# Optimization experiments

Measured on AMD Instinct MI355X. Metric: run time of the kernel, lower is better.

The kernel has to match this reference:

```python
import jax, jax.numpy as jnp
import numpy as np

B, S, H, HEADS = 4, 2048, 512, 8
DK = H // HEADS
LN_EPS = 1e-5
NEG_INF = -1e30


def setup_inputs() -> dict:
    key = jax.random.key(0)
    k = jax.random.split(key, 6)
    x = jax.random.normal(k[0], (B, S, H), dtype=jnp.float32)
    mask = jax.random.randint(k[1], (B, S), 0, 2, dtype=jnp.int32)
    # per-head Q/K/V projection weights stacked: [heads, H, dk]
    Wq = jax.random.normal(k[2], (HEADS, H, DK), dtype=jnp.float32) * 0.05
    Wk = jax.random.normal(k[3], (HEADS, H, DK), dtype=jnp.float32) * 0.05
    Wv = jax.random.normal(k[4], (HEADS, H, DK), dtype=jnp.float32) * 0.05
    # output projection: [heads*dk, H] (y = h @ Wo)
    Wo = jax.random.normal(k[5], (HEADS * DK, H), dtype=jnp.float32) * 0.05
    gamma = jnp.ones((H,), dtype=jnp.float32)
    beta = jnp.zeros((H,), dtype=jnp.float32)
    return {"x": x, "mask": mask, "Wq": Wq, "Wk": Wk, "Wv": Wv,
            "Wo": Wo, "gamma": gamma, "beta": beta}


def reference(x, mask, Wq, Wk, Wv, Wo, gamma, beta):
    # LayerNorm over hidden dim
    mu = jnp.mean(x, axis=-1, keepdims=True)
    var = jnp.mean(jnp.square(x - mu), axis=-1, keepdims=True)
    xn = (x - mu) * jax.lax.rsqrt(var + LN_EPS) * gamma + beta  # [B,S,H]

    mf = mask.astype(jnp.float32)  # [B,S]

    # batched per-head projections (original loops over heads)
    q = jnp.einsum('bsh,nhd->bnsd', xn, Wq)  # [B,heads,S,dk]
    kk = jnp.einsum('bsh,nhd->bnsd', xn, Wk)
    v = jnp.einsum('bsh,nhd->bnsd', xn, Wv)

    scores = jnp.einsum('bnqd,bnkd->bnqk', q, kk) / np.sqrt(DK).astype(np.float32)
    m = mf[:, None, None, :]  # [B,1,1,S] broadcast over query dim
    logits = m * scores + (1.0 - m) * NEG_INF
    probs = jax.nn.softmax(logits, axis=-1)
    attn = jnp.einsum('bnqk,bnkd->bnqd', probs, v)  # [B,heads,S,dk]

    h = attn.transpose(0, 2, 1, 3).reshape(x.shape[0], x.shape[1], HEADS * DK)
    out = h @ Wo + xn          # residual adds post-norm x (as in original)
    out = out * mf[:, :, None]  # zero out masked positions
    return out
```

## Files before the change

kernel.cpp:

```cpp
#include <hip/hip_runtime.h>
#include <hip/hip_bf16.h>
#include <math.h>

#define B_ 4
#define S_ 2048
#define H_ 512
#define HEADS_ 8
#define DK_ 64
#define NROWS_ (B_*S_)
#define LN_EPS_ 1e-5f
#define NEG_INF_ -1e30f
#define QSCALE_ (0.125f * 1.44269504088896f)

typedef short s8v __attribute__((ext_vector_type(8)));
typedef short s4v __attribute__((ext_vector_type(4)));
typedef float f4v __attribute__((ext_vector_type(4)));

typedef __attribute__((address_space(1))) unsigned int gu32_t;
typedef __attribute__((address_space(3))) unsigned int lu32_t;

__device__ __forceinline__ unsigned short f2bf(float f) {
    unsigned int u = __float_as_uint(f);
    u += 0x7FFFu + ((u >> 16) & 1u);
    return (unsigned short)(u >> 16);
}

__device__ __forceinline__ float bf2f(unsigned short u) {
    return __uint_as_float((unsigned int)u << 16);
}

__device__ __forceinline__ s4v pk4bf(float a, float b, float c, float d) {
    union { __hip_bfloat162 h[2]; s4v v; } u;
    u.h[0] = __float22bfloat162_rn(float2{a, b});
    u.h[1] = __float22bfloat162_rn(float2{c, d});
    return u.v;
}

__global__ __launch_bounds__(256) void prep_kernel(
        const float* __restrict__ x, const float* __restrict__ gamma,
        const float* __restrict__ beta, const int* __restrict__ mask,
        const float* __restrict__ Wq, const float* __restrict__ Wk,
        const float* __restrict__ Wv, const float* __restrict__ Wo,
        unsigned short* __restrict__ xnb, float* __restrict__ mb,
        unsigned short* __restrict__ Wt) {
    int bx = blockIdx.x;
    if (bx < 2048) {
        int row  = bx * 4 + (threadIdx.x >> 6);
        int lane = threadIdx.x & 63;
        const float4* xr = (const float4*)(x + (size_t)row * H_ + lane * 8);
        float4 a = xr[0], d = xr[1];
        float s  = (a.x + a.y) + (a.z + a.w) + (d.x + d.y) + (d.z + d.w);
        float ss = (a.x*a.x + a.y*a.y) + (a.z*a.z + a.w*a.w)
                 + (d.x*d.x + d.y*d.y) + (d.z*d.z + d.w*d.w);
        #pragma unroll
        for (int i = 1; i < 64; i <<= 1) {
            s  += __shfl_xor(s, i, 64);
            ss += __shfl_xor(ss, i, 64);
        }
        float mu  = s * (1.f / 512.f);
        float var = ss * (1.f / 512.f) - mu * mu;
        float rstd = rsqrtf(var + LN_EPS_);
        if (lane == 0) mb[row] = mask[row] ? 0.f : NEG_INF_;
        const float4* gp = (const float4*)(gamma + lane * 8);
        const float4* bp = (const float4*)(beta + lane * 8);
        float4 g0 = gp[0], g1 = gp[1], b0 = bp[0], b1 = bp[1];
        float4 y0, y1;
        y0.x = (a.x - mu) * rstd * g0.x + b0.x;
        y0.y = (a.y - mu) * rstd * g0.y + b0.y;
        y0.z = (a.z - mu) * rstd * g0.z + b0.z;
        y0.w = (a.w - mu) * rstd * g0.w + b0.w;
        y1.x = (d.x - mu) * rstd * g1.x + b1.x;
        y1.y = (d.y - mu) * rstd * g1.y + b1.y;
        y1.z = (d.z - mu) * rstd * g1.z + b1.z;
        y1.w = (d.w - mu) * rstd * g1.w + b1.w;
        union { s4v h[2]; s8v v; } pk;
        pk.h[0] = pk4bf(y0.x, y0.y, y0.z, y0.w);
        pk.h[1] = pk4bf(y1.x, y1.y, y1.z, y1.w);
        *(s8v*)(xnb + (size_t)row * H_ + lane * 8) = pk.v;
    } else {
        __shared__ float tile[32][33];
        int wid = bx - 2048;
        const float* src;
        int ld, drow, k0, c0;
        float scale = 1.f;
        if (wid < 768) {
            int z = wid >> 5, rem = wid & 31;
            int cx = rem & 1, ky = rem >> 1;
            k0 = ky * 32; c0 = cx * 32;
            int zw = z >> 3, head = z & 7;
            const float* W = (zw == 0) ? Wq : (zw == 1) ? Wk : Wv;
            if (zw == 0) scale = QSCALE_;
            src = W + (size_t)head * H_ * DK_;
            ld = DK_;
            drow = zw * 512 + head * 64;
        } else {
            int rem = wid - 768;
            int cx = rem & 15, ky = rem >> 4;
            k0 = ky * 32; c0 = cx * 32;
            src = Wo; ld = H_; drow = 1536;
        }
        int tx = threadIdx.x & 31, ty = threadIdx.x >> 5;
        #pragma unroll
        for (int i = 0; i < 4; i++)
            tile[ty * 4 + i][tx] = src[(size_t)(k0 + ty * 4 + i) * ld + c0 + tx];
        __syncthreads();
        #pragma unroll
        for (int i = 0; i < 4; i++) {
            int cc = ty * 4 + i;
            Wt[(size_t)(drow + c0 + cc) * 512 + k0 + tx] = f2bf(tile[tx][cc] * scale);
        }
    }
}

__device__ __forceinline__ void gemm_tile(
        const unsigned short* __restrict__ A,
        const unsigned short* __restrict__ Bt,
        int r0, int j0, f4v acc[4][4]) {
    __shared__ unsigned short As[3 * 128 * 32];
    __shared__ unsigned short Bs[3 * 128 * 32];
    int t = threadIdx.x;
    int wv = t >> 6, L = t & 63, c = L & 15, g = L >> 4;
    int m_base = (wv & 1) * 64, n_base = (wv >> 1) * 64;
    #pragma unroll
    for (int i = 0; i < 4; i++)
        #pragma unroll
        for (int j = 0; j < 4; j++) acc[i][j] = (f4v){0.f, 0.f, 0.f, 0.f};

    auto stage = [&](int buf, int k0) {
        #pragma unroll
        for (int i = 0; i < 2; i++) {
            int uu = wv * 128 + i * 64 + L;
            int row = uu >> 2, k16 = uu & 3;
            __builtin_amdgcn_global_load_lds(
                (const gu32_t*)(A + (size_t)(r0 + row) * 512 + k0 + k16 * 8),
                (lu32_t*)(As + buf * 4096 + (size_t)(wv * 128 + i * 64) * 8), 16, 0, 0);
            __builtin_amdgcn_global_load_lds(
                (const gu32_t*)(Bt + (size_t)(j0 + row) * 512 + k0 + k16 * 8),
                (lu32_t*)(Bs + buf * 4096 + (size_t)(wv * 128 + i * 64) * 8), 16, 0, 0);
        }
    };

    auto compute = [&](int buf) {
        s8v a[4], b[4];
        #pragma unroll
        for (int i = 0; i < 4; i++)
            a[i] = *(const s8v*)(As + buf * 4096 + (size_t)(m_base + i * 16 + c) * 32 + g * 8);
        #pragma unroll
        for (int j = 0; j < 4; j++)
            b[j] = *(const s8v*)(Bs + buf * 4096 + (size_t)(n_base + j * 16 + c) * 32 + g * 8);
        #pragma unroll
        for (int i = 0; i < 4; i++)
            #pragma unroll
            for (int j = 0; j < 4; j++)
                acc[i][j] = __builtin_amdgcn_mfma_f32_16x16x32_bf16(
                    a[i], b[j], acc[i][j], 0, 0, 0);
    };

    stage(0, 0);
    stage(1, 32);
    #pragma unroll
    for (int s = 0; s < 14; ++s) {
        stage((s + 2) % 3, (s + 2) * 32);
        __asm__ volatile("s_waitcnt vmcnt(8)" ::: "memory");
        __builtin_amdgcn_s_barrier();
        compute(s % 3);
        __builtin_amdgcn_s_barrier();
    }
    __asm__ volatile("s_waitcnt vmcnt(4)" ::: "memory");
    __builtin_amdgcn_s_barrier();
    compute(14 % 3);
    __builtin_amdgcn_s_barrier();
    __asm__ volatile("s_waitcnt vmcnt(0)" ::: "memory");
    __builtin_amdgcn_s_barrier();
    compute(15 % 3);
}

__global__ __launch_bounds__(256) void qkv_gemm(
        const unsigned short* __restrict__ xnb,
        const unsigned short* __restrict__ Wt,
        unsigned short* __restrict__ Qb, unsigned short* __restrict__ Kf,
        unsigned short* __restrict__ Vf) {
    f4v acc[4][4];
    int t = threadIdx.x;
    int wv = t >> 6, L = t & 63, c = L & 15, g = L >> 4;
    int rb = wv & 1, cb = wv >> 1;
    if (blockIdx.x < 8) {
        int m0 = blockIdx.x * 128, n0 = blockIdx.y * 128;
        gemm_tile(Wt, xnb, m0, n0, acc);
        int R0 = m0 + rb * 64;
        int C0 = n0 + cb * 64;
        int hd = (R0 >> 6) & 7;
        int b  = C0 >> 11, srow0 = C0 & 2047;
        size_t bhbase = (size_t)(b * HEADS_ + hd) * S_ * DK_;
        if (R0 < 512) {
            #pragma unroll
            for (int msub = 0; msub < 4; msub++) {
                int dk4 = msub * 16 + g * 4;
                #pragma unroll
                for (int nsub = 0; nsub < 4; nsub++) {
                    int tok = srow0 + nsub * 16 + c;
                    s4v v = pk4bf(acc[msub][nsub][0], acc[msub][nsub][1],
                                  acc[msub][nsub][2], acc[msub][nsub][3]);
                    *(s4v*)(Qb + bhbase + (size_t)tok * DK_ + dk4) = v;
                }
            }
        } else {
            unsigned short* dst = Kf + bhbase + (size_t)(srow0 >> 6) * 4096;
            #pragma unroll
            for (int msub = 0; msub < 4; msub++) {
                int gx = (msub & 1) * 2 + (g >> 1);
                int slotbase = (g & 1) * 4 + (msub >> 1) * 8;
                #pragma unroll
                for (int nsub = 0; nsub < 4; nsub++) {
                    s4v v = pk4bf(acc[msub][nsub][0], acc[msub][nsub][1],
                                  acc[msub][nsub][2], acc[msub][nsub][3]);
                    *(s4v*)(dst + nsub * 1024 + (gx * 16 + c) * 16 + slotbase) = v;
                }
            }
        }
    } else {
        int r0 = blockIdx.y * 128, j0 = 1024 + (blockIdx.x - 8) * 128;
        gemm_tile(xnb, Wt, r0, j0, acc);
        int R0 = r0 + rb * 64;
        int C0 = j0 + cb * 64;
        int hd = (C0 >> 6) & 7;
        int b = R0 >> 11, srow0 = R0 & 2047;
        unsigned short* dst = Vf + (size_t)(b * HEADS_ + hd) * S_ * DK_
                              + (size_t)(srow0 >> 6) * 4096;
        #pragma unroll
        for (int msub = 0; msub < 4; msub++)
            #pragma unroll
            for (int nsub = 0; nsub < 4; nsub++) {
                s4v v = pk4bf(acc[msub][nsub][0], acc[msub][nsub][1],
                              acc[msub][nsub][2], acc[msub][nsub][3]);
                *(s4v*)(dst + nsub * 1024 + (g * 16 + c) * 16 + msub * 4) = v;
            }
    }
}

struct KHalf {
    s8v k0lo, k0hi, k1lo, k1hi;
    float4 mb0, mb1;
};

__global__ __launch_bounds__(256, 3) void attn_kernel(
        const unsigned short* __restrict__ Qb,
        const unsigned short* __restrict__ Kf,
        const unsigned short* __restrict__ Vf,
        const float* __restrict__ mb,
        unsigned short* __restrict__ hb) {
    __shared__ float red[2][64][2][17];

    int wv   = threadIdx.x >> 6;
    int qsub = wv & 1;
    int kp   = wv >> 1;
    int L  = threadIdx.x & 63;
    int c  = L & 15;
    int g  = L >> 4;

    unsigned wgid = blockIdx.x + blockIdx.y * 32u;
    unsigned xcd  = wgid & 7u;
    unsigned idx  = wgid >> 3;
    int bh = (int)(xcd + (idx >> 5) * 8u);
    int qt = (int)(idx & 31u);
    int b  = bh >> 3, n = bh & 7;
    int q0 = qt * 64 + qsub * 32;

    const unsigned short* Qbase = Qb + (size_t)bh * S_ * DK_;
    const unsigned short* Kp = Kf + (size_t)bh * S_ * DK_ + (size_t)kp * 16 * 4096 + L * 16;
    const unsigned short* Vp = Vf + (size_t)bh * S_ * DK_ + (size_t)kp * 16 * 4096 + L * 16;
    const float* mbrow = mb + b * S_ + kp * 1024;

    s8v qfA0 = *(const s8v*)(Qbase + (size_t)(q0 + c) * DK_ + g * 8);
    s8v qfA1 = *(const s8v*)(Qbase + (size_t)(q0 + c) * DK_ + 32 + g * 8);
    s8v qfB0 = *(const s8v*)(Qbase + (size_t)(q0 + 16 + c) * DK_ + g * 8);
    s8v qfB1 = *(const s8v*)(Qbase + (size_t)(q0 + 16 + c) * DK_ + 32 + g * 8);

    f4v accA[4], accB[4];
    #pragma unroll
    for (int i = 0; i < 4; i++) {
        accA[i] = (f4v){0.f, 0.f, 0.f, 0.f};
        accB[i] = (f4v){0.f, 0.f, 0.f, 0.f};
    }
    float lacA[4] = {0.f, 0.f, 0.f, 0.f};
    float lacB[4] = {0.f, 0.f, 0.f, 0.f};

    auto load_kh = [&](int kb, int h, KHalf& d) {
        const unsigned short* Kn = Kp + (size_t)kb * 4096;
        d.k0lo = *(const s8v*)(Kn + (h * 2 + 0) * 1024);
        d.k0hi = *(const s8v*)(Kn + (h * 2 + 0) * 1024 + 8);
        d.k1lo = *(const s8v*)(Kn + (h * 2 + 1) * 1024);
        d.k1hi = *(const s8v*)(Kn + (h * 2 + 1) * 1024 + 8);
        d.mb0  = *(const float4*)(mbrow + kb * 64 + h * 32 + g * 4);
        d.mb1  = *(const float4*)(mbrow + kb * 64 + h * 32 + 16 + g * 4);
    };

    auto compute_half = [&](const KHalf& d, int kb, int h) {
        const unsigned short* Vn = Vp + (size_t)kb * 4096;
        s8v vv[4];
        #pragma unroll
        for (int ds = 0; ds < 4; ds++)
            vv[ds] = *(const s8v*)(Vn + ds * 1024 + h * 8);
        f4v bias0 = (f4v){d.mb0.x, d.mb0.y, d.mb0.z, d.mb0.w};
        f4v bias1 = (f4v){d.mb1.x, d.mb1.y, d.mb1.z, d.mb1.w};
        f4v sA0 = bias0, sA1 = bias1, sB0 = bias0, sB1 = bias1;
        sA0 = __builtin_amdgcn_mfma_f32_16x16x32_bf16(d.k0lo, qfA0, sA0, 0, 0, 0);
        sA0 = __builtin_amdgcn_mfma_f32_16x16x32_bf16(d.k0hi, qfA1, sA0, 0, 0, 0);
        sA1 = __builtin_amdgcn_mfma_f32_16x16x32_bf16(d.k1lo, qfA0, sA1, 0, 0, 0);
        sA1 = __builtin_amdgcn_mfma_f32_16x16x32_bf16(d.k1hi, qfA1, sA1, 0, 0, 0);
        sB0 = __builtin_amdgcn_mfma_f32_16x16x32_bf16(d.k0lo, qfB0, sB0, 0, 0, 0);
        sB0 = __builtin_amdgcn_mfma_f32_16x16x32_bf16(d.k0hi, qfB1, sB0, 0, 0, 0);
        sB1 = __builtin_amdgcn_mfma_f32_16x16x32_bf16(d.k1lo, qfB0, sB1, 0, 0, 0);
        sB1 = __builtin_amdgcn_mfma_f32_16x16x32_bf16(d.k1hi, qfB1, sB1, 0, 0, 0);
        float pA0[4], pA1[4], pB0[4], pB1[4];
        #pragma unroll
        for (int r = 0; r < 4; r++) {
            pA0[r] = __builtin_amdgcn_exp2f(sA0[r]);
            pA1[r] = __builtin_amdgcn_exp2f(sA1[r]);
            pB0[r] = __builtin_amdgcn_exp2f(sB0[r]);
            pB1[r] = __builtin_amdgcn_exp2f(sB1[r]);
            lacA[r] += pA0[r] + pA1[r];
            lacB[r] += pB0[r] + pB1[r];
        }
        s4v pfA0 = pk4bf(pA0[0], pA0[1], pA0[2], pA0[3]);
        s4v pfA1 = pk4bf(pA1[0], pA1[1], pA1[2], pA1[3]);
        s4v pfB0 = pk4bf(pB0[0], pB0[1], pB0[2], pB0[3]);
        s4v pfB1 = pk4bf(pB1[0], pB1[1], pB1[2], pB1[3]);
        #pragma unroll
        for (int ds = 0; ds < 4; ds++) {
            s4v v0 = __builtin_shufflevector(vv[ds], vv[ds], 0, 1, 2, 3);
            s4v v1 = __builtin_shufflevector(vv[ds], vv[ds], 4, 5, 6, 7);
            accA[ds] = __builtin_amdgcn_mfma_f32_16x16x16bf16_1k(v0, pfA0, accA[ds], 0, 0, 0);
            accA[ds] = __builtin_amdgcn_mfma_f32_16x16x16bf16_1k(v1, pfA1, accA[ds], 0, 0, 0);
            accB[ds] = __builtin_amdgcn_mfma_f32_16x16x16bf16_1k(v0, pfB0, accB[ds], 0, 0, 0);
            accB[ds] = __builtin_amdgcn_mfma_f32_16x16x16bf16_1k(v1, pfB1, accB[ds], 0, 0, 0);
        }
    };

    KHalf ha, hb2;
    load_kh(0, 0, ha);
    for (int kb = 0; kb < 16; kb++) {
        load_kh(kb, 1, hb2);
        compute_half(ha, kb, 0);
        int kbn = (kb < 15) ? kb + 1 : 15;
        load_kh(kbn, 0, ha);
        compute_half(hb2, kb, 1);
    }

    float lA = (lacA[0] + lacA[1]) + (lacA[2] + lacA[3]);
    float lB = (lacB[0] + lacB[1]) + (lacB[2] + lacB[3]);
    lA += __shfl_xor(lA, 16, 64);
    lA += __shfl_xor(lA, 32, 64);
    lB += __shfl_xor(lB, 16, 64);
    lB += __shfl_xor(lB, 32, 64);

    if (kp == 1) {
        #pragma unroll
        for (int d = 0; d < 4; d++) {
            #pragma unroll
            for (int r = 0; r < 4; r++) {
                red[qsub][L][0][d * 4 + r] = accA[d][r];
                red[qsub][L][1][d * 4 + r] = accB[d][r];
            }
        }
        red[qsub][L][0][16] = lA;
        red[qsub][L][1][16] = lB;
    }
    __syncthreads();
    if (kp == 0) {
        const float* srcA = &red[qsub][L][0][0];
        const float* srcB = &red[qsub][L][1][0];
        float invA = 1.f / (lA + srcA[16]);
        float invB = 1.f / (lB + srcB[16]);
        unsigned short* hpA = hb + (size_t)(b * S_ + q0 + c) * H_ + n * DK_ + g * 4;
        unsigned short* hpB = hpA + (size_t)16 * H_;
        #pragma unroll
        for (int ds = 0; ds < 4; ds++) {
            s4v oA = pk4bf((accA[ds][0] + srcA[ds * 4 + 0]) * invA,
                           (accA[ds][1] + srcA[ds * 4 + 1]) * invA,
                           (accA[ds][2] + srcA[ds * 4 + 2]) * invA,
                           (accA[ds][3] + srcA[ds * 4 + 3]) * invA);
            *(s4v*)(hpA + ds * 16) = oA;
            s4v oB = pk4bf((accB[ds][0] + srcB[ds * 4 + 0]) * invB,
                           (accB[ds][1] + srcB[ds * 4 + 1]) * invB,
                           (accB[ds][2] + srcB[ds * 4 + 2]) * invB,
                           (accB[ds][3] + srcB[ds * 4 + 3]) * invB);
            *(s4v*)(hpB + ds * 16) = oB;
        }
    }
}

__global__ __launch_bounds__(256) void out_gemm(
        const unsigned short* __restrict__ hb,
        const unsigned short* __restrict__ Wot,
        const unsigned short* __restrict__ xnb, const int* __restrict__ mask,
        float* __restrict__ out) {
    f4v acc[4][4];
    int r0 = blockIdx.y * 128, j0 = blockIdx.x * 128;
    gemm_tile(hb, Wot, r0, j0, acc);
    int t = threadIdx.x;
    int wv = t >> 6, L = t & 63, c = L & 15, g = L >> 4;
    int mrow = r0 + (wv & 1) * 64 + g * 4;
    int ncol = j0 + (wv >> 1) * 64 + c;
    #pragma unroll
    for (int msub = 0; msub < 4; msub++) {
        #pragma unroll
        for (int rr = 0; rr < 4; rr++) {
            int row = mrow + msub * 16 + rr;
            float mf = (float)mask[row];
            #pragma unroll
            for (int nsub = 0; nsub < 4; nsub++) {
                int col = ncol + nsub * 16;
                size_t o = (size_t)row * H_ + col;
                out[o] = (acc[msub][nsub][rr] + bf2f(xnb[o])) * mf;
            }
        }
    }
}

extern "C" void kernel_launch(void* const* d_in, const int* in_sizes, int n_in,
                              void* d_out, int out_size, void* d_ws, size_t ws_size,
                              hipStream_t stream) {
    const float* x     = (const float*)d_in[0];
    const int*   mask  = (const int*)d_in[1];
    const float* Wq    = (const float*)d_in[2];
    const float* Wk    = (const float*)d_in[3];
    const float* Wv    = (const float*)d_in[4];
    const float* Wo    = (const float*)d_in[5];
    const float* gamma = (const float*)d_in[6];
    const float* beta  = (const float*)d_in[7];
    float* out = (float*)d_out;

    size_t nelem = (size_t)NROWS_ * H_;
    char* ws = (char*)d_ws;
    unsigned short* xnb = (unsigned short*)ws; ws += nelem * 2;
    unsigned short* hb  = (unsigned short*)ws; ws += nelem * 2;
    unsigned short* Qb  = (unsigned short*)ws; ws += nelem * 2;
    unsigned short* Kf  = (unsigned short*)ws; ws += nelem * 2;
    unsigned short* Vf  = (unsigned short*)ws; ws += nelem * 2;
    unsigned short* Wt  = (unsigned short*)ws; ws += (size_t)2048 * 512 * 2;
    float*          mbp = (float*)ws;

    prep_kernel<<<3072, 256, 0, stream>>>(
        x, gamma, beta, mask, Wq, Wk, Wv, Wo, xnb, mbp, Wt);
    qkv_gemm<<<dim3(12, 64), 256, 0, stream>>>(xnb, Wt, Qb, Kf, Vf);
    attn_kernel<<<dim3(S_ / 64, B_ * HEADS_), 256, 0, stream>>>(
        Qb, Kf, Vf, mbp, hb);
    out_gemm<<<dim3(4, 64), 256, 0, stream>>>(
        hb, Wt + (size_t)1536 * 512, xnb, mask, out);
}
```

Measured before the change: 180.1 us.

## Prefetch V with K in double-buffered attention loop, add MFMA priority hints

The attention loop now prefetches the V fragments together with the K and mask fragments one half-block ahead, instead of loading V at the start of each compute step. MFMA sections are wrapped in s_setprio to raise wave priority during matrix work. Launch bounds drop from 3 to 2 waves per SIMD to make room for the extra prefetch registers. This trades occupancy for more latency hiding of global loads.

After: 174.6 us. 3.0% less time.

```diff
diff --git a/kernel.cpp b/kernel.cpp
--- a/kernel.cpp
+++ b/kernel.cpp
@@ -238,12 +238,82 @@
     }
 }
 
-struct KHalf {
-    s8v k0lo, k0hi, k1lo, k1hi;
-    float4 mb0, mb1;
-};
-
-__global__ __launch_bounds__(256, 3) void attn_kernel(
+#define LOAD_KVH(pfx, hh) do {                                             \
+    int kb_ = (hh) >> 1, h_ = (hh) & 1;                                    \
+    const unsigned short* Kn_ = Kp + (size_t)kb_ * 4096;                   \
+    const unsigned short* Vn_ = Vp + (size_t)kb_ * 4096;                   \
+    pfx##k0lo = *(const s8v*)(Kn_ + (h_ * 2 + 0) * 1024);                  \
+    pfx##k0hi = *(const s8v*)(Kn_ + (h_ * 2 + 0) * 1024 + 8);              \
+    pfx##k1lo = *(const s8v*)(Kn_ + (h_ * 2 + 1) * 1024);                  \
+    pfx##k1hi = *(const s8v*)(Kn_ + (h_ * 2 + 1) * 1024 + 8);              \
+    pfx##mb0  = *(const float4*)(mbrow + kb_ * 64 + h_ * 32 + g * 4);      \
+    pfx##mb1  = *(const float4*)(mbrow + kb_ * 64 + h_ * 32 + 16 + g * 4); \
+    pfx##v0 = *(const s8v*)(Vn_ + 0 * 1024 + h_ * 8);                      \
+    pfx##v1 = *(const s8v*)(Vn_ + 1 * 1024 + h_ * 8);                      \
+    pfx##v2 = *(const s8v*)(Vn_ + 2 * 1024 + h_ * 8);                      \
+    pfx##v3 = *(const s8v*)(Vn_ + 3 * 1024 + h_ * 8);                      \
+} while (0)
+
+#define COMPUTE_HALF(pfx) do {                                                   \
+    f4v bias0 = (f4v){pfx##mb0.x, pfx##mb0.y, pfx##mb0.z, pfx##mb0.w};           \
+    f4v bias1 = (f4v){pfx##mb1.x, pfx##mb1.y, pfx##mb1.z, pfx##mb1.w};           \
+    f4v sA0 = bias0, sA1 = bias1, sB0 = bias0, sB1 = bias1;                      \
+    __builtin_amdgcn_s_setprio(1);                                               \
+    sA0 = __builtin_amdgcn_mfma_f32_16x16x32_bf16(pfx##k0lo, qfA0, sA0, 0, 0, 0);\
+    sA0 = __builtin_amdgcn_mfma_f32_16x16x32_bf16(pfx##k0hi, qfA1, sA0, 0, 0, 0);\
+    sA1 = __builtin_amdgcn_mfma_f32_16x16x32_bf16(pfx##k1lo, qfA0, sA1, 0, 0, 0);\
+    sA1 = __builtin_amdgcn_mfma_f32_16x16x32_bf16(pfx##k1hi, qfA1, sA1, 0, 0, 0);\
+    sB0 = __builtin_amdgcn_mfma_f32_16x16x32_bf16(pfx##k0lo, qfB0, sB0, 0, 0, 0);\
+    sB0 = __builtin_amdgcn_mfma_f32_16x16x32_bf16(pfx##k0hi, qfB1, sB0, 0, 0, 0);\
+    sB1 = __builtin_amdgcn_mfma_f32_16x16x32_bf16(pfx##k1lo, qfB0, sB1, 0, 0, 0);\
+    sB1 = __builtin_amdgcn_mfma_f32_16x16x32_bf16(pfx##k1hi, qfB1, sB1, 0, 0, 0);\
+    __builtin_amdgcn_s_setprio(0);                                               \
+    float pA0[4], pA1[4], pB0[4], pB1[4];                                        \
+    _Pragma("unroll")                                                            \
+    for (int r = 0; r < 4; r++) {                                                \
+        pA0[r] = __builtin_amdgcn_exp2f(sA0[r]);                                 \
+        pA1[r] = __builtin_amdgcn_exp2f(sA1[r]);                                 \
+        pB0[r] = __builtin_amdgcn_exp2f(sB0[r]);                                 \
+        pB1[r] = __builtin_amdgcn_exp2f(sB1[r]);                                 \
+        lacA[r] += pA0[r] + pA1[r];                                              \
+        lacB[r] += pB0[r] + pB1[r];                                              \
+    }                                                                            \
+    s4v pfA0 = pk4bf(pA0[0], pA0[1], pA0[2], pA0[3]);                            \
+    s4v pfA1 = pk4bf(pA1[0], pA1[1], pA1[2], pA1[3]);                            \
+    s4v pfB0 = pk4bf(pB0[0], pB0[1], pB0[2], pB0[3]);                            \
+    s4v pfB1 = pk4bf(pB1[0], pB1[1], pB1[2], pB1[3]);                            \
+    __builtin_amdgcn_s_setprio(1);                                               \
+    {                                                                            \
+        s4v v0, v1;                                                             \
+        v0 = __builtin_shufflevector(pfx##v0, pfx##v0, 0, 1, 2, 3);             \
+        v1 = __builtin_shufflevector(pfx##v0, pfx##v0, 4, 5, 6, 7);             \
+        accA[0] = __builtin_amdgcn_mfma_f32_16x16x16bf16_1k(v0, pfA0, accA[0], 0, 0, 0); \
+        accA[0] = __builtin_amdgcn_mfma_f32_16x16x16bf16_1k(v1, pfA1, accA[0], 0, 0, 0); \
+        accB[0] = __builtin_amdgcn_mfma_f32_16x16x16bf16_1k(v0, pfB0, accB[0], 0, 0, 0); \
+        accB[0] = __builtin_amdgcn_mfma_f32_16x16x16bf16_1k(v1, pfB1, accB[0], 0, 0, 0); \
+        v0 = __builtin_shufflevector(pfx##v1, pfx##v1, 0, 1, 2, 3);             \
+        v1 = __builtin_shufflevector(pfx##v1, pfx##v1, 4, 5, 6, 7);             \
+        accA[1] = __builtin_amdgcn_mfma_f32_16x16x16bf16_1k(v0, pfA0, accA[1], 0, 0, 0); \
+        accA[1] = __builtin_amdgcn_mfma_f32_16x16x16bf16_1k(v1, pfA1, accA[1], 0, 0, 0); \
+        accB[1] = __builtin_amdgcn_mfma_f32_16x16x16bf16_1k(v0, pfB0, accB[1], 0, 0, 0); \
+        accB[1] = __builtin_amdgcn_mfma_f32_16x16x16bf16_1k(v1, pfB1, accB[1], 0, 0, 0); \
+        v0 = __builtin_shufflevector(pfx##v2, pfx##v2, 0, 1, 2, 3);             \
+        v1 = __builtin_shufflevector(pfx##v2, pfx##v2, 4, 5, 6, 7);             \
+        accA[2] = __builtin_amdgcn_mfma_f32_16x16x16bf16_1k(v0, pfA0, accA[2], 0, 0, 0); \
+        accA[2] = __builtin_amdgcn_mfma_f32_16x16x16bf16_1k(v1, pfA1, accA[2], 0, 0, 0); \
+        accB[2] = __builtin_amdgcn_mfma_f32_16x16x16bf16_1k(v0, pfB0, accB[2], 0, 0, 0); \
+        accB[2] = __builtin_amdgcn_mfma_f32_16x16x16bf16_1k(v1, pfB1, accB[2], 0, 0, 0); \
+        v0 = __builtin_shufflevector(pfx##v3, pfx##v3, 0, 1, 2, 3);             \
+        v1 = __builtin_shufflevector(pfx##v3, pfx##v3, 4, 5, 6, 7);             \
+        accA[3] = __builtin_amdgcn_mfma_f32_16x16x16bf16_1k(v0, pfA0, accA[3], 0, 0, 0); \
+        accA[3] = __builtin_amdgcn_mfma_f32_16x16x16bf16_1k(v1, pfA1, accA[3], 0, 0, 0); \
+        accB[3] = __builtin_amdgcn_mfma_f32_16x16x16bf16_1k(v0, pfB0, accB[3], 0, 0, 0); \
+        accB[3] = __builtin_amdgcn_mfma_f32_16x16x16bf16_1k(v1, pfB1, accB[3], 0, 0, 0); \
+    }                                                                            \
+    __builtin_amdgcn_s_setprio(0);                                               \
+} while (0)
+
+__global__ __launch_bounds__(256, 2) void attn_kernel(
         const unsigned short* __restrict__ Qb,
         const unsigned short* __restrict__ Kf,
         const unsigned short* __restrict__ Vf,
@@ -285,66 +355,17 @@
     float lacA[4] = {0.f, 0.f, 0.f, 0.f};
     float lacB[4] = {0.f, 0.f, 0.f, 0.f};
 
-    auto load_kh = [&](int kb, int h, KHalf& d) {
-        const unsigned short* Kn = Kp + (size_t)kb * 4096;
-        d.k0lo = *(const s8v*)(Kn + (h * 2 + 0) * 1024);
-        d.k0hi = *(const s8v*)(Kn + (h * 2 + 0) * 1024 + 8);
-        d.k1lo = *(const s8v*)(Kn + (h * 2 + 1) * 1024);
-        d.k1hi = *(const s8v*)(Kn + (h * 2 + 1) * 1024 + 8);
-        d.mb0  = *(const float4*)(mbrow + kb * 64 + h * 32 + g * 4);
-        d.mb1  = *(const float4*)(mbrow + kb * 64 + h * 32 + 16 + g * 4);
-    };
-
-    auto compute_half = [&](const KHalf& d, int kb, int h) {
-        const unsigned short* Vn = Vp + (size_t)kb * 4096;
-        s8v vv[4];
-        #pragma unroll
-        for (int ds = 0; ds < 4; ds++)
-            vv[ds] = *(const s8v*)(Vn + ds * 1024 + h * 8);
-        f4v bias0 = (f4v){d.mb0.x, d.mb0.y, d.mb0.z, d.mb0.w};
-        f4v bias1 = (f4v){d.mb1.x, d.mb1.y, d.mb1.z, d.mb1.w};
-        f4v sA0 = bias0, sA1 = bias1, sB0 = bias0, sB1 = bias1;
-        sA0 = __builtin_amdgcn_mfma_f32_16x16x32_bf16(d.k0lo, qfA0, sA0, 0, 0, 0);
-        sA0 = __builtin_amdgcn_mfma_f32_16x16x32_bf16(d.k0hi, qfA1, sA0, 0, 0, 0);
-        sA1 = __builtin_amdgcn_mfma_f32_16x16x32_bf16(d.k1lo, qfA0, sA1, 0, 0, 0);
-        sA1 = __builtin_amdgcn_mfma_f32_16x16x32_bf16(d.k1hi, qfA1, sA1, 0, 0, 0);
-        sB0 = __builtin_amdgcn_mfma_f32_16x16x32_bf16(d.k0lo, qfB0, sB0, 0, 0, 0);
-        sB0 = __builtin_amdgcn_mfma_f32_16x16x32_bf16(d.k0hi, qfB1, sB0, 0, 0, 0);
-        sB1 = __builtin_amdgcn_mfma_f32_16x16x32_bf16(d.k1lo, qfB0, sB1, 0, 0, 0);
-        sB1 = __builtin_amdgcn_mfma_f32_16x16x32_bf16(d.k1hi, qfB1, sB1, 0, 0, 0);
-        float pA0[4], pA1[4], pB0[4], pB1[4];
-        #pragma unroll
-        for (int r = 0; r < 4; r++) {
-            pA0[r] = __builtin_amdgcn_exp2f(sA0[r]);
-            pA1[r] = __builtin_amdgcn_exp2f(sA1[r]);
-            pB0[r] = __builtin_amdgcn_exp2f(sB0[r]);
-            pB1[r] = __builtin_amdgcn_exp2f(sB1[r]);
-            lacA[r] += pA0[r] + pA1[r];
-            lacB[r] += pB0[r] + pB1[r];
-        }
-        s4v pfA0 = pk4bf(pA0[0], pA0[1], pA0[2], pA0[3]);
-        s4v pfA1 = pk4bf(pA1[0], pA1[1], pA1[2], pA1[3]);
-        s4v pfB0 = pk4bf(pB0[0], pB0[1], pB0[2], pB0[3]);
-        s4v pfB1 = pk4bf(pB1[0], pB1[1], pB1[2], pB1[3]);
-        #pragma unroll
-        for (int ds = 0; ds < 4; ds++) {
-            s4v v0 = __builtin_shufflevector(vv[ds], vv[ds], 0, 1, 2, 3);
-            s4v v1 = __builtin_shufflevector(vv[ds], vv[ds], 4, 5, 6, 7);
-            accA[ds] = __builtin_amdgcn_mfma_f32_16x16x16bf16_1k(v0, pfA0, accA[ds], 0, 0, 0);
-            accA[ds] = __builtin_amdgcn_mfma_f32_16x16x16bf16_1k(v1, pfA1, accA[ds], 0, 0, 0);
-            accB[ds] = __builtin_amdgcn_mfma_f32_16x16x16bf16_1k(v0, pfB0, accB[ds], 0, 0, 0);
-            accB[ds] = __builtin_amdgcn_mfma_f32_16x16x16bf16_1k(v1, pfB1, accB[ds], 0, 0, 0);
-        }
-    };
-
-    KHalf ha, hb2;
-    load_kh(0, 0, ha);
-    for (int kb = 0; kb < 16; kb++) {
-        load_kh(kb, 1, hb2);
-        compute_half(ha, kb, 0);
-        int kbn = (kb < 15) ? kb + 1 : 15;
-        load_kh(kbn, 0, ha);
-        compute_half(hb2, kb, 1);
+    s8v a_k0lo, a_k0hi, a_k1lo, a_k1hi, a_v0, a_v1, a_v2, a_v3;
+    float4 a_mb0, a_mb1;
+    s8v b_k0lo, b_k0hi, b_k1lo, b_k1hi, b_v0, b_v1, b_v2, b_v3;
+    float4 b_mb0, b_mb1;
+
+    LOAD_KVH(a_, 0);
+    for (int hh = 0; hh < 32; hh += 2) {
+        LOAD_KVH(b_, hh + 1);
+        COMPUTE_HALF(a_);
+        if (hh + 2 < 32) LOAD_KVH(a_, hh + 2);
+        COMPUTE_HALF(b_);
     }
 
     float lA = (lacA[0] + lacA[1]) + (lacA[2] + lacA[3]);
```
